# Optimization experiments

Hardware: AMD Instinct MI355X
Metric: run time of the kernel (lower is better)

Reference implementation:

```python
import jax, jax.numpy as jnp
import numpy as np

N = 100000
E = 1600000
F_IN = 64
HID = 64
OUT = 64


def _sage_conv(x, src, dst, w_l, b_l, w_r):
    # PyG SAGEConv (mean aggr): out = lin_l(mean_{j in N(i)} x_j) + lin_r(x_i)
    msgs = x[src]                                             # [E, F] gather
    summed = jax.ops.segment_sum(msgs, dst, num_segments=N)   # [N, F]
    ones = jnp.ones((src.shape[0],), dtype=x.dtype)
    cnt = jax.ops.segment_sum(ones, dst, num_segments=N)      # [N]
    mean = summed / jnp.maximum(cnt, 1.0)[:, None]
    return mean @ w_l + b_l + x @ w_r


def setup_inputs() -> dict:
    key = jax.random.key(0)
    ks = jax.random.split(key, 12)
    sc = lambda f: 1.0 / np.sqrt(f)
    inp = {
        "h": jax.random.normal(ks[0], (N, F_IN), dtype=jnp.float32),
        "edge_index": jax.random.randint(ks[1], (2, E), 0, N, dtype=jnp.int64),
        # conv1: lin_l (with bias) and lin_r (no bias), weights stored [in, out]
        "w1_l": jax.random.normal(ks[2], (F_IN, HID), dtype=jnp.float32) * sc(F_IN),
        "b1_l": jnp.zeros((HID,), dtype=jnp.float32),
        "w1_r": jax.random.normal(ks[3], (F_IN, HID), dtype=jnp.float32) * sc(F_IN),
        "w_lin1": jax.random.normal(ks[4], (HID, HID), dtype=jnp.float32) * sc(HID),
        "b_lin1": jnp.zeros((HID,), dtype=jnp.float32),
        "w2_l": jax.random.normal(ks[5], (HID, HID), dtype=jnp.float32) * sc(HID),
        "b2_l": jnp.zeros((HID,), dtype=jnp.float32),
        "w2_r": jax.random.normal(ks[6], (HID, HID), dtype=jnp.float32) * sc(HID),
        "w_lin2": jax.random.normal(ks[7], (HID, OUT), dtype=jnp.float32) * sc(HID),
        "b_lin2": jnp.zeros((OUT,), dtype=jnp.float32),
    }
    return inp


def reference(h, edge_index, w1_l, b1_l, w1_r, w_lin1, b_lin1,
              w2_l, b2_l, w2_r, w_lin2, b_lin2):
    src, dst = edge_index[0], edge_index[1]
    x = jax.nn.relu(_sage_conv(h, src, dst, w1_l, b1_l, w1_r))
    x = jax.nn.relu(x @ w_lin1 + b_lin1)
    x = jax.nn.relu(_sage_conv(x, src, dst, w2_l, b2_l, w2_r))
    x = x @ w_lin2 + b_lin2
    return x
```

## Files before the change

### kernel.cpp

```cpp
#include <hip/hip_runtime.h>
#include <hip/hip_fp16.h>

#define FEAT   64
#define BSHIFT 8
#define BNODES 256
#define MAXB   512
#define CHUNK  4096
#define REGION 5120

typedef _Float16 half8 __attribute__((ext_vector_type(8)));
typedef float  float4v __attribute__((ext_vector_type(4)));

__global__ __launch_bounds__(256) void setup_kernel(
    const float* __restrict__ h, __half* __restrict__ h16, int n4, int CB,
    const float* w0, const float* w1, const float* w2,
    const float* w3, const float* w4, const float* w5,
    __half* __restrict__ wT, int* __restrict__ bcur)
{
    int b = blockIdx.x;
    if (b < CB) {
        int i = b * 256 + threadIdx.x;
        if (i < n4) {
            float4 v = ((const float4*)h)[i];
            union { uint2 u; __half2 h2[2]; } r;
            r.h2[0] = __floats2half2_rn(v.x, v.y);
            r.h2[1] = __floats2half2_rn(v.z, v.w);
            ((uint2*)h16)[i] = r.u;
        }
    } else if (b < CB + 96) {
        int bb = b - CB;
        int m = bb >> 4;
        int idx = ((bb & 15) << 8) | threadIdx.x;
        const float* src = m==0?w0 : m==1?w1 : m==2?w2 : m==3?w3 : m==4?w4 : w5;
        int o = idx >> 6, i = idx & 63;
        wT[m * 4096 + o * 64 + i] = __float2half(src[i * 64 + o]);
    } else {
        bcur[threadIdx.x] = 0;
        bcur[threadIdx.x + 256] = 0;
    }
}

__global__ __launch_bounds__(512) void partition_kernel(
    const int* __restrict__ src, const int* __restrict__ dst,
    int* __restrict__ bcur, int* __restrict__ pedge, int E)
{
    __shared__ int cnt[MAXB];
    __shared__ int sa[MAXB], sb[MAXB];
    __shared__ int gb[MAXB];
    __shared__ int lcur[MAXB];
    __shared__ int stage[CHUNK];
    __shared__ int tgt[CHUNK];

    int tid = threadIdx.x;
    cnt[tid] = 0;
    __syncthreads();

    int base = blockIdx.x * CHUNK;
    int vals[8];
    int bs[8];
#pragma unroll
    for (int i = 0; i < 8; i++) {
        int e = base + tid + i * 512;
        bs[i] = -1;
        if (e < E) {
            int s_ = src[e];
            int d_ = dst[e];
            int b  = d_ >> BSHIFT;
            bs[i]  = b;
            vals[i] = s_ | ((d_ & (BNODES - 1)) << 20);
            atomicAdd(&cnt[b], 1);
        }
    }
    __syncthreads();

    sa[tid] = cnt[tid];
    __syncthreads();
    int* cur = sa; int* nxt = sb;
    for (int off = 1; off < MAXB; off <<= 1) {
        nxt[tid] = cur[tid] + ((tid >= off) ? cur[tid - off] : 0);
        __syncthreads();
        int* tmp = cur; cur = nxt; nxt = tmp;
    }
    {
        int c = cnt[tid];
        int lo = cur[tid] - c;
        int gbase = c ? atomicAdd(&bcur[tid], c) : 0;
        if (gbase > REGION) gbase = REGION;
        gb[tid]   = tid * REGION + gbase - lo;
        lcur[tid] = lo;
    }
    __syncthreads();

#pragma unroll
    for (int i = 0; i < 8; i++) {
        if (bs[i] >= 0) {
            int pos = atomicAdd(&lcur[bs[i]], 1);
            stage[pos] = vals[i];
            tgt[pos]   = gb[bs[i]];
        }
    }
    __syncthreads();

    int cn = min(CHUNK, E - base);
    for (int i = tid; i < cn; i += 512)
        pedge[tgt[i] + i] = stage[i];
}

__global__ __launch_bounds__(512) void buildcsr_kernel(
    const int* __restrict__ pedge, const int* __restrict__ bcur,
    unsigned* __restrict__ rowinfo, int* __restrict__ csr, int N)
{
    __shared__ int stg[REGION];
    __shared__ int srt[REGION];
    __shared__ int hist[BNODES], scn[BNODES], lcur[BNODES];
    int b = blockIdx.x;
    int tid = threadIdx.x;
    int beg = b * REGION;
    int cnt = min(bcur[b], REGION);

    if (tid < BNODES) hist[tid] = 0;
    __syncthreads();

    for (int i = tid; i < cnt; i += 512) {
        int p = pedge[beg + i];
        stg[i] = p;
        atomicAdd(&hist[p >> 20], 1);
    }
    __syncthreads();

    int v = 0;
    if (tid < BNODES) { v = hist[tid]; scn[tid] = v; }
    __syncthreads();
    for (int off = 1; off < BNODES; off <<= 1) {
        int t = 0;
        if (tid < BNODES && tid >= off) t = scn[tid - off];
        __syncthreads();
        if (tid < BNODES) scn[tid] += t;
        __syncthreads();
    }
    if (tid < BNODES) {
        int excl = scn[tid] - v;
        int node = (b << BSHIFT) + tid;
        if (node < N)
            rowinfo[node] = (unsigned)(beg + excl) | ((unsigned)v << 21);
        lcur[tid] = excl;
    }
    __syncthreads();

    for (int i = tid; i < cnt; i += 512) {
        int p = stg[i];
        int pos = atomicAdd(&lcur[p >> 20], 1);
        srt[pos] = p & 0xFFFFF;
    }
    __syncthreads();
    for (int i = tid; i < cnt; i += 512)
        csr[beg + i] = srt[i];
}

__global__ __launch_bounds__(256) void fused_layer_kernel(
    const __half* __restrict__ x, const unsigned* __restrict__ rowinfo,
    const int* __restrict__ csr_src,
    const __half* __restrict__ wlT, const __half* __restrict__ wrT,
    const __half* __restrict__ w2T,
    const float* __restrict__ b1, const float* __restrict__ b2,
    float* __restrict__ out_f, __half* __restrict__ out_h,
    int n, int relu_out)
{
    __shared__ __attribute__((aligned(16))) _Float16 sbuf[64][72];

    int tid  = threadIdx.x;
    int wave = tid >> 6;
    int lane = tid & 63;
    int sg   = tid >> 4;
    int gg   = (tid >> 3) & 1;
    int s8   = tid & 7;
    int r    = lane & 15;
    int q    = lane >> 4;
    int base = blockIdx.x * 64 + wave * 16;

    int arow = min(base + r, n - 1);
    const half8* xrow = (const half8*)(x + (size_t)arow * FEAT);
    half8 Ax0 = xrow[q], Ax1 = xrow[4 + q];

    unsigned infos[4];
#pragma unroll
    for (int i = 0; i < 4; i++) {
        int node = blockIdx.x * 64 + sg * 4 + i;
        infos[i] = (node < n) ? rowinfo[node] : 0u;
    }

    int beg4[4], deg4[4];
    int itmax = 0;
#pragma unroll
    for (int i = 0; i < 4; i++) {
        beg4[i] = (int)(infos[i] & 0x1FFFFFu);
        deg4[i] = (int)(infos[i] >> 21);
        int it = (deg4[i] + 3) >> 2;
        itmax = max(itmax, it);
    }
    float acc[4][8];
#pragma unroll
    for (int i = 0; i < 4; i++)
#pragma unroll
        for (int t = 0; t < 8; t++) acc[i][t] = 0.f;

    int  c0[4], c1[4];
    bool p0[4], p1[4];
#pragma unroll
    for (int i = 0; i < 4; i++) {
        int be = beg4[i] + gg;
        int en = beg4[i] + deg4[i];
        p0[i] = be < en;
        p1[i] = be + 2 < en;
        c0[i] = csr_src[p0[i] ? be : beg4[i]];
        c1[i] = csr_src[p1[i] ? be + 2 : beg4[i]];
    }

    for (int it = 0; it < itmax; ++it) {
        int  n0[4], n1[4];
        bool m0[4], m1[4];
#pragma unroll
        for (int i = 0; i < 4; i++) {
            int be = beg4[i] + gg + (it + 1) * 4;
            int en = beg4[i] + deg4[i];
            m0[i] = be < en;
            m1[i] = be + 2 < en;
            n0[i] = csr_src[m0[i] ? be : beg4[i]];
            n1[i] = csr_src[m1[i] ? be + 2 : beg4[i]];
        }
#pragma unroll
        for (int i = 0; i < 4; i++) {
            int j0 = p0[i] ? c0[i] : 0;
            int j1 = p1[i] ? c1[i] : 0;
            union { uint4 u; __half2 h2[4]; } r0, r1;
            r0.u = ((const uint4*)(x + (size_t)j0 * FEAT))[s8];
            r1.u = ((const uint4*)(x + (size_t)j1 * FEAT))[s8];
            float w0 = p0[i] ? 1.0f : 0.0f;
            float w1 = p1[i] ? 1.0f : 0.0f;
#pragma unroll
            for (int t = 0; t < 4; t++) {
                float2 f0 = __half22float2(r0.h2[t]);
                float2 f1 = __half22float2(r1.h2[t]);
                acc[i][2*t]   = fmaf(w0, f0.x, acc[i][2*t]);
                acc[i][2*t]   = fmaf(w1, f1.x, acc[i][2*t]);
                acc[i][2*t+1] = fmaf(w0, f0.y, acc[i][2*t+1]);
                acc[i][2*t+1] = fmaf(w1, f1.y, acc[i][2*t+1]);
            }
        }
#pragma unroll
        for (int i = 0; i < 4; i++) {
            c0[i] = n0[i]; c1[i] = n1[i];
            p0[i] = m0[i]; p1[i] = m1[i];
        }
    }

#pragma unroll
    for (int i = 0; i < 4; i++) {
#pragma unroll
        for (int t = 0; t < 8; t++)
            acc[i][t] += __shfl_xor(acc[i][t], 8, 64);
        if (gg == 0) {
            int deg = deg4[i];
            float inv = deg ? 1.0f / (float)deg : 0.0f;
            union { uint4 u; __half2 h2[4]; } o;
            o.h2[0] = __floats2half2_rn(acc[i][0]*inv, acc[i][1]*inv);
            o.h2[1] = __floats2half2_rn(acc[i][2]*inv, acc[i][3]*inv);
            o.h2[2] = __floats2half2_rn(acc[i][4]*inv, acc[i][5]*inv);
            o.h2[3] = __floats2half2_rn(acc[i][6]*inv, acc[i][7]*inv);
            int ln = sg * 4 + i;
            *(uint4*)&sbuf[ln][s8 * 8] = o.u;
        }
    }
    __syncthreads();

    union { uint4 u4; half8 h; } Am0u, Am1u;
    Am0u.u4 = *(const uint4*)&sbuf[wave * 16 + r][q * 8];
    Am1u.u4 = *(const uint4*)&sbuf[wave * 16 + r][(4 + q) * 8];

    float4v acc1[4];
#pragma unroll
    for (int c = 0; c < 4; c++) {
        float bv = b1[c * 16 + r];
        acc1[c] = (float4v){bv, bv, bv, bv};
        const half8* bl = (const half8*)(wlT + (size_t)(c * 16 + r) * FEAT);
        const half8* br = (const half8*)(wrT + (size_t)(c * 16 + r) * FEAT);
        acc1[c] = __builtin_amdgcn_mfma_f32_16x16x32_f16(Am0u.h, bl[q],     acc1[c], 0, 0, 0);
        acc1[c] = __builtin_amdgcn_mfma_f32_16x16x32_f16(Am1u.h, bl[4 + q], acc1[c], 0, 0, 0);
        acc1[c] = __builtin_amdgcn_mfma_f32_16x16x32_f16(Ax0,    br[q],     acc1[c], 0, 0, 0);
        acc1[c] = __builtin_amdgcn_mfma_f32_16x16x32_f16(Ax1,    br[4 + q], acc1[c], 0, 0, 0);
    }
#pragma unroll
    for (int c = 0; c < 4; c++)
#pragma unroll
        for (int t = 0; t < 4; t++)
            sbuf[wave * 16 + q * 4 + t][c * 16 + r] = (_Float16)fmaxf(acc1[c][t], 0.0f);
    __syncthreads();

    union { uint4 u4; half8 h; } A2[2];
#pragma unroll
    for (int s = 0; s < 2; s++)
        A2[s].u4 = *(const uint4*)&sbuf[wave * 16 + r][s * 32 + q * 8];

    float4v acc2[4];
#pragma unroll
    for (int c = 0; c < 4; c++) {
        float bv = b2[c * 16 + r];
        acc2[c] = (float4v){bv, bv, bv, bv};
        const half8* bw = (const half8*)(w2T + (size_t)(c * 16 + r) * FEAT);
        acc2[c] = __builtin_amdgcn_mfma_f32_16x16x32_f16(A2[0].h, bw[q],     acc2[c], 0, 0, 0);
        acc2[c] = __builtin_amdgcn_mfma_f32_16x16x32_f16(A2[1].h, bw[4 + q], acc2[c], 0, 0, 0);
    }

#pragma unroll
    for (int c = 0; c < 4; c++)
#pragma unroll
        for (int t = 0; t < 4; t++) {
            int gr = base + q * 4 + t;
            if (gr < n) {
                float v = acc2[c][t];
                if (relu_out) v = fmaxf(v, 0.0f);
                if (out_h) out_h[(size_t)gr * FEAT + c * 16 + r] = __float2half(v);
                else       out_f[(size_t)gr * FEAT + c * 16 + r] = v;
            }
        }
}

extern "C" void kernel_launch(void* const* d_in, const int* in_sizes, int n_in,
                              void* d_out, int out_size, void* d_ws, size_t ws_size,
                              hipStream_t stream) {
    const float* h      = (const float*)d_in[0];
    const int*   ei     = (const int*)d_in[1];
    const float* w1_l   = (const float*)d_in[2];
    const float* b1_l   = (const float*)d_in[3];
    const float* w1_r   = (const float*)d_in[4];
    const float* w_lin1 = (const float*)d_in[5];
    const float* b_lin1 = (const float*)d_in[6];
    const float* w2_l   = (const float*)d_in[7];
    const float* b2_l   = (const float*)d_in[8];
    const float* w2_r   = (const float*)d_in[9];
    const float* w_lin2 = (const float*)d_in[10];
    const float* b_lin2 = (const float*)d_in[11];

    const int N = in_sizes[0] / FEAT;
    const int E = in_sizes[1] / 2;
    const int* src  = ei;
    const int* dst_ = ei + E;

    const int NB = (N + BNODES - 1) >> BSHIFT;
    const int PB = (E + CHUNK - 1) / CHUNK;
    const int n4 = N * FEAT / 4;
    const int CB = (n4 + 255) / 256;
    const int fblk = (N + 63) / 64;

    size_t off = 0;
    int* bcur       = (int*)d_ws + off; off += MAXB;
    unsigned* rowinfo = (unsigned*)((int*)d_ws + off); off += (size_t)N;
    off = (off + 3) & ~(size_t)3;
    int* csr    = (int*)d_ws + off; off += (size_t)NB * REGION + 64;
    off = (off + 3) & ~(size_t)3;
    __half* h16 = (__half*)((int*)d_ws + off); off += (size_t)N * FEAT / 2;
    __half* x2h = (__half*)((int*)d_ws + off); off += (size_t)N * FEAT / 2;
    __half* wT  = (__half*)((int*)d_ws + off); off += 6 * 2048;
    int* pedge  = (int*)d_ws + off; off += (size_t)NB * REGION;

    setup_kernel<<<CB + 96 + 1, 256, 0, stream>>>(
        h, h16, n4, CB, w1_l, w1_r, w_lin1, w2_l, w2_r, w_lin2, wT, bcur);
    partition_kernel<<<PB, 512, 0, stream>>>(src, dst_, bcur, pedge, E);
    buildcsr_kernel<<<NB, 512, 0, stream>>>(pedge, bcur, rowinfo, csr, N);

    fused_layer_kernel<<<fblk, 256, 0, stream>>>(
        h16, rowinfo, csr,
        wT + 0 * 4096, wT + 1 * 4096, wT + 2 * 4096,
        b1_l, b_lin1, (float*)nullptr, x2h, N, 1);

    fused_layer_kernel<<<fblk, 256, 0, stream>>>(
        x2h, rowinfo, csr,
        wT + 3 * 4096, wT + 4 * 4096, wT + 5 * 4096,
        b2_l, b_lin2, (float*)d_out, (__half*)nullptr, N, 0);
}
```

Measured before the change: 235.0 us.

## Stage block's CSR edge indices in LDS and batch all neighbor gathers per iteration

Each block now loads its contiguous span of CSR source indices (up to 2048) into shared memory cooperatively before aggregation, instead of each thread issuing scattered global loads with register prefetch. The inner loop issues all eight neighbor-row loads first and then accumulates, so more memory requests are in flight at once. Launch bounds request four blocks per SM to limit register use. This adds a syncthreads, about 8KB of extra LDS per block, and a global fallback path for spans beyond the cap.

```diff
diff --git a/kernel.cpp b/kernel.cpp
--- a/kernel.cpp
+++ b/kernel.cpp
@@ -7,6 +7,7 @@
 #define MAXB   512
 #define CHUNK  4096
 #define REGION 5120
+#define ECAP   2048
 
 typedef _Float16 half8 __attribute__((ext_vector_type(8)));
 typedef float  float4v __attribute__((ext_vector_type(4)));
@@ -157,7 +158,7 @@
         csr[beg + i] = srt[i];
 }
 
-__global__ __launch_bounds__(256) void fused_layer_kernel(
+__global__ __launch_bounds__(256, 4) void fused_layer_kernel(
     const __half* __restrict__ x, const unsigned* __restrict__ rowinfo,
     const int* __restrict__ csr_src,
     const __half* __restrict__ wlT, const __half* __restrict__ wrT,
@@ -167,6 +168,7 @@
     int n, int relu_out)
 {
     __shared__ __attribute__((aligned(16))) _Float16 sbuf[64][72];
+    __shared__ int sedge[ECAP];
 
     int tid  = threadIdx.x;
     int wave = tid >> 6;
@@ -177,26 +179,36 @@
     int r    = lane & 15;
     int q    = lane >> 4;
     int base = blockIdx.x * 64 + wave * 16;
+    int node0 = blockIdx.x * 64;
 
     int arow = min(base + r, n - 1);
     const half8* xrow = (const half8*)(x + (size_t)arow * FEAT);
     half8 Ax0 = xrow[q], Ax1 = xrow[4 + q];
 
+    unsigned i0 = rowinfo[node0];
+    unsigned iL = rowinfo[min(node0 + 63, n - 1)];
+    int beg0 = (int)(i0 & 0x1FFFFFu);
+    int span = (int)(iL & 0x1FFFFFu) + (int)(iL >> 21) - beg0;
+
     unsigned infos[4];
 #pragma unroll
     for (int i = 0; i < 4; i++) {
-        int node = blockIdx.x * 64 + sg * 4 + i;
+        int node = node0 + sg * 4 + i;
         infos[i] = (node < n) ? rowinfo[node] : 0u;
     }
 
-    int beg4[4], deg4[4];
+    int spanc = min(span, ECAP);
+    for (int i = tid; i < spanc; i += 256)
+        sedge[i] = csr_src[beg0 + i];
+    __syncthreads();
+
+    int lbeg[4], deg4[4];
     int itmax = 0;
 #pragma unroll
     for (int i = 0; i < 4; i++) {
-        beg4[i] = (int)(infos[i] & 0x1FFFFFu);
         deg4[i] = (int)(infos[i] >> 21);
-        int it = (deg4[i] + 3) >> 2;
-        itmax = max(itmax, it);
+        lbeg[i] = deg4[i] ? (int)(infos[i] & 0x1FFFFFu) - beg0 : 0;
+        itmax = max(itmax, (deg4[i] + 3) >> 2);
     }
     float acc[4][8];
 #pragma unroll
@@ -204,53 +216,34 @@
 #pragma unroll
         for (int t = 0; t < 8; t++) acc[i][t] = 0.f;
 
-    int  c0[4], c1[4];
-    bool p0[4], p1[4];
-#pragma unroll
-    for (int i = 0; i < 4; i++) {
-        int be = beg4[i] + gg;
-        int en = beg4[i] + deg4[i];
-        p0[i] = be < en;
-        p1[i] = be + 2 < en;
-        c0[i] = csr_src[p0[i] ? be : beg4[i]];
-        c1[i] = csr_src[p1[i] ? be + 2 : beg4[i]];
-    }
-
     for (int it = 0; it < itmax; ++it) {
-        int  n0[4], n1[4];
-        bool m0[4], m1[4];
+        uint4  rr[8];
+        float  ww[8];
 #pragma unroll
         for (int i = 0; i < 4; i++) {
-            int be = beg4[i] + gg + (it + 1) * 4;
-            int en = beg4[i] + deg4[i];
-            m0[i] = be < en;
-            m1[i] = be + 2 < en;
-            n0[i] = csr_src[m0[i] ? be : beg4[i]];
-            n1[i] = csr_src[m1[i] ? be + 2 : beg4[i]];
-        }
-#pragma unroll
-        for (int i = 0; i < 4; i++) {
-            int j0 = p0[i] ? c0[i] : 0;
-            int j1 = p1[i] ? c1[i] : 0;
-            union { uint4 u; __half2 h2[4]; } r0, r1;
-            r0.u = ((const uint4*)(x + (size_t)j0 * FEAT))[s8];
-            r1.u = ((const uint4*)(x + (size_t)j1 * FEAT))[s8];
-            float w0 = p0[i] ? 1.0f : 0.0f;
-            float w1 = p1[i] ? 1.0f : 0.0f;
+            int o0 = (it << 2) + gg;
+            int o1 = o0 + 2;
+            bool v0 = o0 < deg4[i];
+            bool v1 = o1 < deg4[i];
+            int l0 = lbeg[i] + (v0 ? o0 : 0);
+            int l1 = lbeg[i] + (v1 ? o1 : 0);
+            int j0 = v0 ? ((l0 < ECAP) ? sedge[l0] : csr_src[beg0 + l0]) : 0;
+            int j1 = v1 ? ((l1 < ECAP) ? sedge[l1] : csr_src[beg0 + l1]) : 0;
+            rr[2*i]   = ((const uint4*)(x + (size_t)j0 * FEAT))[s8];
+            rr[2*i+1] = ((const uint4*)(x + (size_t)j1 * FEAT))[s8];
+            ww[2*i]   = v0 ? 1.0f : 0.0f;
+            ww[2*i+1] = v1 ? 1.0f : 0.0f;
+        }
+#pragma unroll
+        for (int k = 0; k < 8; k++) {
+            union { uint4 u; __half2 h2[4]; } rv; rv.u = rr[k];
+            int a = k >> 1;
 #pragma unroll
             for (int t = 0; t < 4; t++) {
-                float2 f0 = __half22float2(r0.h2[t]);
-                float2 f1 = __half22float2(r1.h2[t]);
-                acc[i][2*t]   = fmaf(w0, f0.x, acc[i][2*t]);
-                acc[i][2*t]   = fmaf(w1, f1.x, acc[i][2*t]);
-                acc[i][2*t+1] = fmaf(w0, f0.y, acc[i][2*t+1]);
-                acc[i][2*t+1] = fmaf(w1, f1.y, acc[i][2*t+1]);
+                float2 f = __half22float2(rv.h2[t]);
+                acc[a][2*t]   = fmaf(ww[k], f.x, acc[a][2*t]);
+                acc[a][2*t+1] = fmaf(ww[k], f.y, acc[a][2*t+1]);
             }
-        }
-#pragma unroll
-        for (int i = 0; i < 4; i++) {
-            c0[i] = n0[i]; c1[i] = n1[i];
-            p0[i] = m0[i]; p1[i] = m1[i];
         }
     }
 
```

Measured after the change: 237.7 us. Within noise of the previous version (+1.1%).

## Merge setup and partition kernels into one prep launch, add occupancy hint

Applied to the files above, without the earlier changes.

Combines the fp16 conversion of node features and the weight transposes into the same launch as the edge partition kernel, using extra blocks past the partition range. The bucket counter reset moves to a memset so the partition blocks can run without a preceding kernel. This removes one launch and its serialization gap and lets the conversion overlap with partitioning. It also adds a minimum-blocks-per-CU hint to the fused layer kernel, which may limit its register use. The conversion blocks now reserve the partition kernel's large shared memory, which can lower their occupancy.

```diff
diff --git a/kernel.cpp b/kernel.cpp
--- a/kernel.cpp
+++ b/kernel.cpp
@@ -11,38 +11,14 @@
 typedef _Float16 half8 __attribute__((ext_vector_type(8)));
 typedef float  float4v __attribute__((ext_vector_type(4)));
 
-__global__ __launch_bounds__(256) void setup_kernel(
-    const float* __restrict__ h, __half* __restrict__ h16, int n4, int CB,
+__global__ __launch_bounds__(512) void prep_kernel(
+    const int* __restrict__ esrc, const int* __restrict__ edst,
+    int* __restrict__ bcur, int* __restrict__ pedge, int E, int PB,
+    const float* __restrict__ h, __half* __restrict__ h16,
+    int n4, int CVB,
     const float* w0, const float* w1, const float* w2,
     const float* w3, const float* w4, const float* w5,
-    __half* __restrict__ wT, int* __restrict__ bcur)
-{
-    int b = blockIdx.x;
-    if (b < CB) {
-        int i = b * 256 + threadIdx.x;
-        if (i < n4) {
-            float4 v = ((const float4*)h)[i];
-            union { uint2 u; __half2 h2[2]; } r;
-            r.h2[0] = __floats2half2_rn(v.x, v.y);
-            r.h2[1] = __floats2half2_rn(v.z, v.w);
-            ((uint2*)h16)[i] = r.u;
-        }
-    } else if (b < CB + 96) {
-        int bb = b - CB;
-        int m = bb >> 4;
-        int idx = ((bb & 15) << 8) | threadIdx.x;
-        const float* src = m==0?w0 : m==1?w1 : m==2?w2 : m==3?w3 : m==4?w4 : w5;
-        int o = idx >> 6, i = idx & 63;
-        wT[m * 4096 + o * 64 + i] = __float2half(src[i * 64 + o]);
-    } else {
-        bcur[threadIdx.x] = 0;
-        bcur[threadIdx.x + 256] = 0;
-    }
-}
-
-__global__ __launch_bounds__(512) void partition_kernel(
-    const int* __restrict__ src, const int* __restrict__ dst,
-    int* __restrict__ bcur, int* __restrict__ pedge, int E)
+    __half* __restrict__ wT)
 {
     __shared__ int cnt[MAXB];
     __shared__ int sa[MAXB], sb[MAXB];
@@ -51,11 +27,35 @@
     __shared__ int stage[CHUNK];
     __shared__ int tgt[CHUNK];
 
+    int b   = blockIdx.x;
     int tid = threadIdx.x;
+
+    if (b >= PB) {
+        int bb = b - PB;
+        if (bb < CVB) {
+            int i = bb * 512 + tid;
+            if (i < n4) {
+                float4 v = ((const float4*)h)[i];
+                union { uint2 u; __half2 h2[2]; } r;
+                r.h2[0] = __floats2half2_rn(v.x, v.y);
+                r.h2[1] = __floats2half2_rn(v.z, v.w);
+                ((uint2*)h16)[i] = r.u;
+            }
+        } else {
+            int idx = (bb - CVB) * 512 + tid;
+            int m = idx >> 12;
+            int e = idx & 4095;
+            const float* src = m==0?w0 : m==1?w1 : m==2?w2 : m==3?w3 : m==4?w4 : w5;
+            int o = e >> 6, i = e & 63;
+            wT[m * 4096 + o * 64 + i] = __float2half(src[i * 64 + o]);
+        }
+        return;
+    }
+
     cnt[tid] = 0;
     __syncthreads();
 
-    int base = blockIdx.x * CHUNK;
+    int base = b * CHUNK;
     int vals[8];
     int bs[8];
 #pragma unroll
@@ -63,12 +63,12 @@
         int e = base + tid + i * 512;
         bs[i] = -1;
         if (e < E) {
-            int s_ = src[e];
-            int d_ = dst[e];
-            int b  = d_ >> BSHIFT;
-            bs[i]  = b;
+            int s_ = esrc[e];
+            int d_ = edst[e];
+            int bk = d_ >> BSHIFT;
+            bs[i]  = bk;
             vals[i] = s_ | ((d_ & (BNODES - 1)) << 20);
-            atomicAdd(&cnt[b], 1);
+            atomicAdd(&cnt[bk], 1);
         }
     }
     __syncthreads();
@@ -157,7 +157,7 @@
         csr[beg + i] = srt[i];
 }
 
-__global__ __launch_bounds__(256) void fused_layer_kernel(
+__global__ __launch_bounds__(256, 4) void fused_layer_kernel(
     const __half* __restrict__ x, const unsigned* __restrict__ rowinfo,
     const int* __restrict__ csr_src,
     const __half* __restrict__ wlT, const __half* __restrict__ wrT,
@@ -346,10 +346,10 @@
     const int* src  = ei;
     const int* dst_ = ei + E;
 
-    const int NB = (N + BNODES - 1) >> BSHIFT;
-    const int PB = (E + CHUNK - 1) / CHUNK;
-    const int n4 = N * FEAT / 4;
-    const int CB = (n4 + 255) / 256;
+    const int NB  = (N + BNODES - 1) >> BSHIFT;
+    const int PB  = (E + CHUNK - 1) / CHUNK;
+    const int n4  = N * FEAT / 4;
+    const int CVB = (n4 + 511) / 512;
     const int fblk = (N + 63) / 64;
 
     size_t off = 0;
@@ -363,9 +363,11 @@
     __half* wT  = (__half*)((int*)d_ws + off); off += 6 * 2048;
     int* pedge  = (int*)d_ws + off; off += (size_t)NB * REGION;
 
-    setup_kernel<<<CB + 96 + 1, 256, 0, stream>>>(
-        h, h16, n4, CB, w1_l, w1_r, w_lin1, w2_l, w2_r, w_lin2, wT, bcur);
-    partition_kernel<<<PB, 512, 0, stream>>>(src, dst_, bcur, pedge, E);
+    hipMemsetAsync(bcur, 0, MAXB * sizeof(int), stream);
+    prep_kernel<<<PB + CVB + 48, 512, 0, stream>>>(
+        src, dst_, bcur, pedge, E, PB,
+        h, h16, n4, CVB,
+        w1_l, w1_r, w_lin1, w2_l, w2_r, w_lin2, wT);
     buildcsr_kernel<<<NB, 512, 0, stream>>>(pedge, bcur, rowinfo, csr, N);
 
     fused_layer_kernel<<<fblk, 256, 0, stream>>>(
```

Measured after the change: 235.2 us. No clear change (+0.1%).
